# Optimization experiments

Hardware: AMD Instinct MI355X
Metric: run time of the kernel (lower is better)

## Reference

```python
import jax, jax.numpy as jnp
import numpy as np

D_MODEL = 1024
NUM_HEADS = 16
DEPTH = D_MODEL // NUM_HEADS
EPS = 1e-6


def setup_inputs() -> dict:
    key = jax.random.key(0)
    ks = jax.random.split(key, 9)
    B, S = 4, 2048
    scale = 1.0 / np.sqrt(D_MODEL)
    inp = {
        "inputs": jax.random.normal(ks[0], (B, S, D_MODEL), dtype=jnp.float32),
        "Wq": jax.random.normal(ks[1], (D_MODEL, D_MODEL), dtype=jnp.float32) * scale,
        "bq": jnp.zeros((D_MODEL,), dtype=jnp.float32),
        "Wk": jax.random.normal(ks[2], (D_MODEL, D_MODEL), dtype=jnp.float32) * scale,
        "bk": jnp.zeros((D_MODEL,), dtype=jnp.float32),
        "Wv": jax.random.normal(ks[3], (D_MODEL, D_MODEL), dtype=jnp.float32) * scale,
        "bv": jnp.zeros((D_MODEL,), dtype=jnp.float32),
        "Wo": jax.random.normal(ks[4], (D_MODEL, D_MODEL), dtype=jnp.float32) * scale,
        "bo": jnp.zeros((D_MODEL,), dtype=jnp.float32),
        "gamma": jnp.ones((D_MODEL,), dtype=jnp.float32),
        "beta": jnp.zeros((D_MODEL,), dtype=jnp.float32),
    }
    return inp


def _layer_norm(x, gamma, beta):
    mu = jnp.mean(x, axis=-1, keepdims=True)
    var = jnp.mean(jnp.square(x - mu), axis=-1, keepdims=True)
    return (x - mu) * jax.lax.rsqrt(var + EPS) * gamma + beta


def reference(inputs, Wq, bq, Wk, bk, Wv, bv, Wo, bo, gamma, beta):
    B, S, _ = inputs.shape
    # QKV projections, split heads: [B, H, S, depth]
    def split_heads(x):
        return x.reshape(B, S, NUM_HEADS, DEPTH).transpose(0, 2, 1, 3)

    q = split_heads(inputs @ Wq + bq)
    k = split_heads(inputs @ Wk + bk)
    v = split_heads(inputs @ Wv + bv)

    # scores: [B, H, S, S]
    scores = jnp.einsum("bhqd,bhkd->bhqk", q, k) / jnp.sqrt(
        jnp.asarray(DEPTH, dtype=inputs.dtype))
    attn = jax.nn.softmax(scores, axis=-1)  # dropout is identity in eval mode
    out = jnp.einsum("bhqk,bhkd->bhqd", attn, v)
    out = out.transpose(0, 2, 1, 3).reshape(B, S, D_MODEL)
    out = out @ Wo + bo  # dropout2 identity in eval mode
    return _layer_norm(inputs + out, gamma, beta)
```

## Files before the change

kernel.cpp:

```cpp
#include <hip/hip_runtime.h>
#include <hip/hip_bf16.h>


typedef __bf16 bf16;
typedef __bf16 bf16x4 __attribute__((ext_vector_type(4)));
typedef __bf16 bf16x8 __attribute__((ext_vector_type(8)));
typedef float floatx4 __attribute__((ext_vector_type(4)));

#define MFMA16(a, b, c) __builtin_amdgcn_mfma_f32_16x16x32_bf16((a), (b), (c), 0, 0, 0)

static __device__ __forceinline__ floatx4 vmax4(floatx4 a, floatx4 b) {
    floatx4 r;
    r[0] = fmaxf(a[0], b[0]); r[1] = fmaxf(a[1], b[1]);
    r[2] = fmaxf(a[2], b[2]); r[3] = fmaxf(a[3], b[3]);
    return r;
}

static __device__ __forceinline__ void gload16(const bf16* g, bf16* lds_base) {
    __builtin_amdgcn_global_load_lds(
        (__attribute__((address_space(1))) void*)(g),
        (__attribute__((address_space(3))) void*)(lds_base), 16, 0, 0);
}

__global__ __launch_bounds__(256) void convert_kernel(
    const float* __restrict__ x, bf16* __restrict__ xb)
{
    const int i = blockIdx.x * 256 + threadIdx.x;
    const float4 v = ((const float4*)x)[i];
    bf16x4 r;
    r[0] = (bf16)v.x; r[1] = (bf16)v.y; r[2] = (bf16)v.z; r[3] = (bf16)v.w;
    ((bf16x4*)xb)[i] = r;
}

__global__ __launch_bounds__(256) void transpose_kernel(
    const float* __restrict__ Wq, const float* __restrict__ Wk,
    const float* __restrict__ Wv, const float* __restrict__ Wo,
    bf16* __restrict__ WT, bf16* __restrict__ WoT)
{
    __shared__ float tile[32][33];
    const int z = blockIdx.z;
    const float* src = (z == 0) ? Wq : (z == 1) ? Wk : (z == 2) ? Wv : Wo;
    bf16* dst = (z < 3) ? (WT + (long)z * 1024 * 1024) : WoT;
    const int n0 = blockIdx.x * 32, k0 = blockIdx.y * 32;
    const int tx = threadIdx.x & 31, ty = threadIdx.x >> 5;
#pragma unroll
    for (int i = 0; i < 32; i += 8)
        tile[ty + i][tx] = src[(long)(k0 + ty + i) * 1024 + n0 + tx];
    __syncthreads();
#pragma unroll
    for (int i = 0; i < 32; i += 8)
        dst[(long)(n0 + ty + i) * 1024 + k0 + tx] = (bf16)tile[tx][ty + i];
}

template <int MODE>
__global__ __launch_bounds__(256, 2) void gemm_kernel(
    const bf16* __restrict__ A, const bf16* __restrict__ Bt,
    const float* __restrict__ b0, const float* __restrict__ b1,
    const float* __restrict__ b2, const float* __restrict__ X,
    bf16* __restrict__ Qo, bf16* __restrict__ Ko, bf16* __restrict__ Vto,
    bf16* __restrict__ Tmpb, int N, int K)
{
    constexpr int LDT = 32;
    constexpr int NBX = (MODE == 0) ? 24 : 8;
    constexpr int NWG = NBX * 64;
    constexpr int CPX = NWG / 8;
    __shared__ __align__(16) bf16 As[2][128 * LDT];
    __shared__ __align__(16) bf16 Bs[2][128 * LDT];
    const int t = threadIdx.x;
    const int lane = t & 63;
    const int w = t >> 6;
    const int wm = w >> 1, wn = w & 1;
    const int g = lane >> 4, c = lane & 15;

    const int id = blockIdx.y * NBX + blockIdx.x;
    const int swz = (id & 7) * CPX + (id >> 3);
    const int bm = (swz / NBX) * 128;
    const int bn = (swz % NBX) * 128;

    const bf16* asrc[2];
    const bf16* bsrc[2];
    int ldsoff[2];
#pragma unroll
    for (int i = 0; i < 2; ++i) {
        const int ch = (i * 4 + w) * 64 + lane;
        const int row = ch >> 2, col = ch & 3;
        asrc[i] = A + (long)(bm + row) * K + col * 8;
        bsrc[i] = Bt + (long)(bn + row) * K + col * 8;
        ldsoff[i] = (i * 4 + w) * 512;
    }

    floatx4 acc[4][4];
#pragma unroll
    for (int i = 0; i < 4; ++i)
#pragma unroll
        for (int j = 0; j < 4; ++j) acc[i][j] = floatx4{0.f, 0.f, 0.f, 0.f};

#pragma unroll
    for (int i = 0; i < 2; ++i) {
        gload16(asrc[i], &As[0][ldsoff[i]]);
        gload16(bsrc[i], &Bs[0][ldsoff[i]]);
    }

    int cur = 0;
    for (int k0 = 0; k0 < K; k0 += 32) {
        __syncthreads();
        if (k0 + 32 < K) {
#pragma unroll
            for (int i = 0; i < 2; ++i) {
                gload16(asrc[i] + k0 + 32, &As[cur ^ 1][ldsoff[i]]);
                gload16(bsrc[i] + k0 + 32, &Bs[cur ^ 1][ldsoff[i]]);
            }
        }
        bf16x8 af[4], bfv[4];
#pragma unroll
        for (int i = 0; i < 4; ++i)
            af[i] = *(const bf16x8*)&As[cur][(wm * 64 + i * 16 + c) * LDT + g * 8];
#pragma unroll
        for (int j = 0; j < 4; ++j)
            bfv[j] = *(const bf16x8*)&Bs[cur][(wn * 64 + j * 16 + c) * LDT + g * 8];
#pragma unroll
        for (int i = 0; i < 4; ++i)
#pragma unroll
            for (int j = 0; j < 4; ++j)
                acc[i][j] = MFMA16(af[i], bfv[j], acc[i][j]);
        cur ^= 1;
    }

    if (MODE == 0) {
#pragma unroll
        for (int j = 0; j < 4; ++j) {
            const int col = bn + wn * 64 + j * 16 + c;
            const int sec = col >> 10;
            const int nn = col & 1023;
            const int h = nn >> 6, dd = nn & 63;
            const float* bp = (sec == 0) ? b0 : (sec == 1) ? b1 : b2;
            const float bias = bp[nn];
#pragma unroll
            for (int i = 0; i < 4; ++i) {
                const int r0 = bm + wm * 64 + i * 16 + g * 4;
                if (sec == 2) {
                    bf16x4 pack;
#pragma unroll
                    for (int reg = 0; reg < 4; ++reg)
                        pack[reg] = (bf16)(acc[i][j][reg] + bias);
                    const int b_ = r0 >> 11, sr = r0 & 2047;
                    *(bf16x4*)&Vto[((long)(b_ * 16 + h) * 64 + dd) * 2048 + sr] = pack;
                } else {
#pragma unroll
                    for (int reg = 0; reg < 4; ++reg) {
                        const int r = r0 + reg;
                        const int b_ = r >> 11, sr = r & 2047;
                        const float v = acc[i][j][reg] + bias;
                        if (sec == 0)
                            Qo[((long)(b_ * 16 + h) * 2048 + sr) * 64 + dd] =
                                (bf16)(v * 0.18033688011112042f);
                        else
                            Ko[((long)(b_ * 16 + h) * 2048 + sr) * 64 + dd] = (bf16)v;
                    }
                }
            }
        }
    } else {
#pragma unroll
        for (int j = 0; j < 4; ++j) {
            const int col = bn + wn * 64 + j * 16 + c;
            const float bias = b0[col];
#pragma unroll
            for (int i = 0; i < 4; ++i) {
#pragma unroll
                for (int reg = 0; reg < 4; ++reg) {
                    const int r = bm + wm * 64 + i * 16 + g * 4 + reg;
                    Tmpb[(long)r * N + col] =
                        (bf16)(acc[i][j][reg] + bias + X[(long)r * N + col]);
                }
            }
        }
    }
}

__global__ __launch_bounds__(256, 2) void flash_kernel(
    const bf16* __restrict__ Q, const bf16* __restrict__ Kc,
    const bf16* __restrict__ Vt, bf16* __restrict__ O)
{
    constexpr int KSTR = 72;
    constexpr int VSTR = 72;
    constexpr int PSTR = 72;
    __shared__ __align__(16) bf16 Ks[64 * KSTR];
    __shared__ __align__(16) bf16 Vs[64 * VSTR];
    __shared__ __align__(16) bf16 Pl[4 * 32 * PSTR];
    const int t = threadIdx.x;
    const int lane = t & 63;
    const int w = t >> 6;
    const int g = lane >> 4, c = lane & 15;
    const int bh = blockIdx.x;
    const int b_ = bh >> 4, h = bh & 15;
    const bf16* Qp = Q + (long)bh * 2048 * 64;
    const bf16* Kp = Kc + (long)bh * 2048 * 64;
    const bf16* Vp = Vt + (long)bh * 64 * 2048;
    const int q0 = blockIdx.y * 128 + w * 32;
    bf16* Pw = Pl + w * 32 * PSTR;

    bf16x8 qf[2][2];
#pragma unroll
    for (int qs = 0; qs < 2; ++qs)
#pragma unroll
        for (int p = 0; p < 2; ++p)
            qf[qs][p] = *(const bf16x8*)(Qp + (long)(q0 + qs * 16 + c) * 64 + p * 32 + g * 8);

    float m_c[2] = {-1e30f, -1e30f};
    float l_c[2] = {0.f, 0.f};
    floatx4 o[2][4];
#pragma unroll
    for (int qs = 0; qs < 2; ++qs)
#pragma unroll
        for (int dd = 0; dd < 4; ++dd) o[qs][dd] = floatx4{0.f, 0.f, 0.f, 0.f};

    for (int kt = 0; kt < 32; ++kt) {
        __syncthreads();
        {
            uint4 kr[2], vr[2];
#pragma unroll
            for (int i = 0; i < 2; ++i) {
                const int idx = i * 256 + t;
                kr[i] = *(const uint4*)(Kp + (long)kt * 4096 + idx * 8);
                vr[i] = *(const uint4*)(Vp + (long)(idx >> 3) * 2048 + kt * 64 + (idx & 7) * 8);
            }
#pragma unroll
            for (int i = 0; i < 2; ++i) {
                const int idx = i * 256 + t;
                *(uint4*)&Ks[(idx >> 3) * KSTR + (idx & 7) * 8] = kr[i];
                *(uint4*)&Vs[(idx >> 3) * VSTR + (idx & 7) * 8] = vr[i];
            }
        }
        __syncthreads();

        floatx4 s[2][4];
#pragma unroll
        for (int ks = 0; ks < 4; ++ks) {
            bf16x8 kf0 = *(const bf16x8*)&Ks[(ks * 16 + c) * KSTR + g * 8];
            bf16x8 kf1 = *(const bf16x8*)&Ks[(ks * 16 + c) * KSTR + 32 + g * 8];
#pragma unroll
            for (int qs = 0; qs < 2; ++qs) {
                floatx4 z = floatx4{0.f, 0.f, 0.f, 0.f};
                z = MFMA16(kf0, qf[qs][0], z);
                z = MFMA16(kf1, qf[qs][1], z);
                s[qs][ks] = z;
            }
        }

#pragma unroll
        for (int qs = 0; qs < 2; ++qs) {
            floatx4 t0 = vmax4(vmax4(s[qs][0], s[qs][1]), vmax4(s[qs][2], s[qs][3]));
            float mx = fmaxf(fmaxf(t0[0], t0[1]), fmaxf(t0[2], t0[3]));
            mx = fmaxf(mx, __shfl_xor(mx, 16, 64));
            mx = fmaxf(mx, __shfl_xor(mx, 32, 64));
            const float mn = fmaxf(m_c[qs], mx);
            const float al = __builtin_amdgcn_exp2f(m_c[qs] - mn);
            m_c[qs] = mn;
            floatx4 a4 = floatx4{0.f, 0.f, 0.f, 0.f};
#pragma unroll
            for (int ks = 0; ks < 4; ++ks) {
#pragma unroll
                for (int r = 0; r < 4; ++r)
                    s[qs][ks][r] = __builtin_amdgcn_exp2f(s[qs][ks][r] - mn);
                a4 += s[qs][ks];
            }
            float rs = (a4[0] + a4[1]) + (a4[2] + a4[3]);
            rs += __shfl_xor(rs, 16, 64);
            rs += __shfl_xor(rs, 32, 64);
            l_c[qs] = l_c[qs] * al + rs;
#pragma unroll
            for (int dd = 0; dd < 4; ++dd)
#pragma unroll
                for (int r = 0; r < 4; ++r) o[qs][dd][r] *= al;
#pragma unroll
            for (int ks = 0; ks < 4; ++ks) {
                bf16x4 pk;
#pragma unroll
                for (int r = 0; r < 4; ++r) pk[r] = (bf16)s[qs][ks][r];
                *(bf16x4*)&Pw[(qs * 16 + c) * PSTR + ks * 16 + g * 4] = pk;
            }
        }
        asm volatile("s_waitcnt lgkmcnt(0)" ::: "memory");
#pragma unroll
        for (int kk = 0; kk < 2; ++kk) {
            bf16x8 pf0 = *(const bf16x8*)&Pw[(0 + c) * PSTR + kk * 32 + g * 8];
            bf16x8 pf1 = *(const bf16x8*)&Pw[(16 + c) * PSTR + kk * 32 + g * 8];
#pragma unroll
            for (int dd = 0; dd < 4; ++dd) {
                bf16x8 vf = *(const bf16x8*)&Vs[(dd * 16 + c) * VSTR + kk * 32 + g * 8];
                o[0][dd] = MFMA16(vf, pf0, o[0][dd]);
                o[1][dd] = MFMA16(vf, pf1, o[1][dd]);
            }
        }
    }

#pragma unroll
    for (int qs = 0; qs < 2; ++qs) {
        const float linv = 1.0f / l_c[qs];
        const int q = q0 + qs * 16 + c;
#pragma unroll
        for (int dd = 0; dd < 4; ++dd) {
            bf16x4 pk;
#pragma unroll
            for (int r = 0; r < 4; ++r) pk[r] = (bf16)(o[qs][dd][r] * linv);
            *(bf16x4*)&O[((long)b_ * 2048 + q) * 1024 + h * 64 + dd * 16 + g * 4] = pk;
        }
    }
}

__global__ __launch_bounds__(256, 2) void ln_kernel(
    const bf16* __restrict__ Tmp, const float* __restrict__ gamma,
    const float* __restrict__ beta, float* __restrict__ out)
{
    const int row = blockIdx.x;
    const int t = threadIdx.x;
    const int lane = t & 63, w = t >> 6;
    const bf16x4 vb = ((const bf16x4*)(Tmp + (long)row * 1024))[t];
    const float xv[4] = {(float)vb[0], (float)vb[1], (float)vb[2], (float)vb[3]};
    float s = xv[0] + xv[1] + xv[2] + xv[3];
    float ss = xv[0] * xv[0] + xv[1] * xv[1] + xv[2] * xv[2] + xv[3] * xv[3];
#pragma unroll
    for (int off = 1; off < 64; off <<= 1) {
        s += __shfl_xor(s, off, 64);
        ss += __shfl_xor(ss, off, 64);
    }
    __shared__ float sb[4], ssb[4];
    if (lane == 0) { sb[w] = s; ssb[w] = ss; }
    __syncthreads();
    s = sb[0] + sb[1] + sb[2] + sb[3];
    ss = ssb[0] + ssb[1] + ssb[2] + ssb[3];
    const float mu = s * (1.0f / 1024.0f);
    const float var = ss * (1.0f / 1024.0f) - mu * mu;
    const float inv = rsqrtf(var + 1e-6f);
    const float4 gm = ((const float4*)gamma)[t];
    const float4 bt = ((const float4*)beta)[t];
    float4 r;
    r.x = (xv[0] - mu) * inv * gm.x + bt.x;
    r.y = (xv[1] - mu) * inv * gm.y + bt.y;
    r.z = (xv[2] - mu) * inv * gm.z + bt.z;
    r.w = (xv[3] - mu) * inv * gm.w + bt.w;
    ((float4*)(out + (long)row * 1024))[t] = r;
}

extern "C" void kernel_launch(void* const* d_in, const int* in_sizes, int n_in,
                              void* d_out, int out_size, void* d_ws, size_t ws_size,
                              hipStream_t stream)
{
    const float* x     = (const float*)d_in[0];
    const float* Wq    = (const float*)d_in[1];
    const float* bq    = (const float*)d_in[2];
    const float* Wk    = (const float*)d_in[3];
    const float* bk    = (const float*)d_in[4];
    const float* Wv    = (const float*)d_in[5];
    const float* bv    = (const float*)d_in[6];
    const float* Wo    = (const float*)d_in[7];
    const float* bo    = (const float*)d_in[8];
    const float* gamma = (const float*)d_in[9];
    const float* beta  = (const float*)d_in[10];
    float* out = (float*)d_out;

    char* ws = (char*)d_ws;
    bf16* xb   = (bf16*)(ws);
    bf16* WT   = (bf16*)(ws + 16777216);
    bf16* Qb   = (bf16*)(ws + 23068672);
    bf16* Kb   = (bf16*)(ws + 39845888);
    bf16* WoT  = (bf16*)(ws + 56623104);
    bf16* Tmpb = (bf16*)(ws);
    bf16* Vtb  = (bf16*)d_out;
    bf16* Ob   = (bf16*)((char*)d_out + 16777216);

    convert_kernel<<<8192, 256, 0, stream>>>(x, xb);
    transpose_kernel<<<dim3(32, 32, 4), 256, 0, stream>>>(Wq, Wk, Wv, Wo, WT, WoT);
    gemm_kernel<0><<<dim3(24, 64), 256, 0, stream>>>(
        xb, WT, bq, bk, bv, nullptr, Qb, Kb, Vtb, nullptr, 3072, 1024);
    flash_kernel<<<dim3(64, 16), 256, 0, stream>>>(Qb, Kb, Vtb, Ob);
    gemm_kernel<1><<<dim3(8, 64), 256, 0, stream>>>(
        Ob, WoT, bo, nullptr, nullptr, x, nullptr, nullptr, nullptr, Tmpb, 1024, 1024);
    ln_kernel<<<8192, 256, 0, stream>>>(Tmpb, gamma, beta, out);
}
```

Measured before the change: 340.1 us.

## Restructure flash attention with 32x32 MFMA, register P, double-buffered async K/V loads

Rewrites the attention kernel to use 32x32x16 bf16 MFMA tiles, so each wave handles 32 query rows with one softmax state. The P matrix is rearranged into the operand layout with cross-half-wave shuffles instead of a round trip through LDS. K/V tiles are now double-buffered and loaded with async global_load_lds into an XOR-swizzled unpadded layout, which overlaps the next tile's load with the current compute and removes one barrier per iteration. The cost is heavier register use for the 16-wide accumulators, and correctness depends on the async loads being complete before the barrier.

Result: faster. 325.0 us (-4.4%).

```diff
diff --git a/kernel.cpp b/kernel.cpp
--- a/kernel.cpp
+++ b/kernel.cpp
@@ -3,18 +3,14 @@
 
 
 typedef __bf16 bf16;
+typedef __bf16 bf16x2 __attribute__((ext_vector_type(2)));
 typedef __bf16 bf16x4 __attribute__((ext_vector_type(4)));
 typedef __bf16 bf16x8 __attribute__((ext_vector_type(8)));
 typedef float floatx4 __attribute__((ext_vector_type(4)));
+typedef float floatx16 __attribute__((ext_vector_type(16)));
 
 #define MFMA16(a, b, c) __builtin_amdgcn_mfma_f32_16x16x32_bf16((a), (b), (c), 0, 0, 0)
-
-static __device__ __forceinline__ floatx4 vmax4(floatx4 a, floatx4 b) {
-    floatx4 r;
-    r[0] = fmaxf(a[0], b[0]); r[1] = fmaxf(a[1], b[1]);
-    r[2] = fmaxf(a[2], b[2]); r[3] = fmaxf(a[3], b[3]);
-    return r;
-}
+#define MFMA32(a, b, c) __builtin_amdgcn_mfma_f32_32x32x16_bf16((a), (b), (c), 0, 0, 0)
 
 static __device__ __forceinline__ void gload16(const bf16* g, bf16* lds_base) {
     __builtin_amdgcn_global_load_lds(
@@ -182,131 +178,167 @@
     const bf16* __restrict__ Q, const bf16* __restrict__ Kc,
     const bf16* __restrict__ Vt, bf16* __restrict__ O)
 {
-    constexpr int KSTR = 72;
-    constexpr int VSTR = 72;
-    constexpr int PSTR = 72;
-    __shared__ __align__(16) bf16 Ks[64 * KSTR];
-    __shared__ __align__(16) bf16 Vs[64 * VSTR];
-    __shared__ __align__(16) bf16 Pl[4 * 32 * PSTR];
+    __shared__ __align__(16) bf16 KVs[2][2][64 * 64];
     const int t = threadIdx.x;
     const int lane = t & 63;
     const int w = t >> 6;
-    const int g = lane >> 4, c = lane & 15;
+    const int l31 = lane & 31, hw = lane >> 5;
     const int bh = blockIdx.x;
     const int b_ = bh >> 4, h = bh & 15;
     const bf16* Qp = Q + (long)bh * 2048 * 64;
     const bf16* Kp = Kc + (long)bh * 2048 * 64;
     const bf16* Vp = Vt + (long)bh * 64 * 2048;
-    const int q0 = blockIdx.y * 128 + w * 32;
-    bf16* Pw = Pl + w * 32 * PSTR;
-
-    bf16x8 qf[2][2];
-#pragma unroll
-    for (int qs = 0; qs < 2; ++qs)
-#pragma unroll
-        for (int p = 0; p < 2; ++p)
-            qf[qs][p] = *(const bf16x8*)(Qp + (long)(q0 + qs * 16 + c) * 64 + p * 32 + g * 8);
-
-    float m_c[2] = {-1e30f, -1e30f};
-    float l_c[2] = {0.f, 0.f};
-    floatx4 o[2][4];
-#pragma unroll
-    for (int qs = 0; qs < 2; ++qs)
-#pragma unroll
-        for (int dd = 0; dd < 4; ++dd) o[qs][dd] = floatx4{0.f, 0.f, 0.f, 0.f};
+    const int q0w = blockIdx.y * 128 + w * 32;
+
+    const bf16* ksrc[2];
+    const bf16* vsrc[2];
+    int ldsoff[2];
+#pragma unroll
+    for (int i = 0; i < 2; ++i) {
+        const int ch = (i * 4 + w) * 64 + lane;
+        const int row = ch >> 3, col = ch & 7;
+        const int sw = col ^ (row & 7);
+        ksrc[i] = Kp + (long)(row * 8 + sw) * 8;
+        vsrc[i] = Vp + (long)row * 2048 + sw * 8;
+        ldsoff[i] = (i * 4 + w) * 512;
+    }
+
+    bf16x8 qf[4];
+#pragma unroll
+    for (int sl = 0; sl < 4; ++sl)
+        qf[sl] = *(const bf16x8*)(Qp + (long)(q0w + l31) * 64 + sl * 16 + hw * 8);
+
+    float m_c = -1e30f;
+    float l_c = 0.f;
+    floatx16 o32[2];
+#pragma unroll
+    for (int dt = 0; dt < 2; ++dt)
+#pragma unroll
+        for (int i = 0; i < 16; ++i) o32[dt][i] = 0.f;
+
+#pragma unroll
+    for (int i = 0; i < 2; ++i) {
+        gload16(ksrc[i], &KVs[0][0][ldsoff[i]]);
+        gload16(vsrc[i], &KVs[0][1][ldsoff[i]]);
+    }
 
     for (int kt = 0; kt < 32; ++kt) {
         __syncthreads();
+        const int cur = kt & 1;
+        if (kt + 1 < 32) {
+#pragma unroll
+            for (int i = 0; i < 2; ++i) {
+                gload16(ksrc[i] + (long)(kt + 1) * 4096, &KVs[cur ^ 1][0][ldsoff[i]]);
+                gload16(vsrc[i] + (long)(kt + 1) * 64,   &KVs[cur ^ 1][1][ldsoff[i]]);
+            }
+        }
+        const bf16* KsB = KVs[cur][0];
+        const bf16* VsB = KVs[cur][1];
+
+        floatx16 s32[2];
+#pragma unroll
+        for (int kt_ = 0; kt_ < 2; ++kt_)
+#pragma unroll
+            for (int i = 0; i < 16; ++i) s32[kt_][i] = 0.f;
+#pragma unroll
+        for (int sl = 0; sl < 4; ++sl) {
+            const int x = sl * 2 + hw;
+            const int r0 = l31, r1 = 32 + l31;
+            const int xs = x ^ (r0 & 7);
+            bf16x8 kf0 = *(const bf16x8*)&KsB[r0 * 64 + (xs << 3)];
+            bf16x8 kf1 = *(const bf16x8*)&KsB[r1 * 64 + (xs << 3)];
+            s32[0] = MFMA32(kf0, qf[sl], s32[0]);
+            s32[1] = MFMA32(kf1, qf[sl], s32[1]);
+        }
+
+        float mx;
         {
-            uint4 kr[2], vr[2];
-#pragma unroll
-            for (int i = 0; i < 2; ++i) {
-                const int idx = i * 256 + t;
-                kr[i] = *(const uint4*)(Kp + (long)kt * 4096 + idx * 8);
-                vr[i] = *(const uint4*)(Vp + (long)(idx >> 3) * 2048 + kt * 64 + (idx & 7) * 8);
-            }
-#pragma unroll
-            for (int i = 0; i < 2; ++i) {
-                const int idx = i * 256 + t;
-                *(uint4*)&Ks[(idx >> 3) * KSTR + (idx & 7) * 8] = kr[i];
-                *(uint4*)&Vs[(idx >> 3) * VSTR + (idx & 7) * 8] = vr[i];
-            }
-        }
-        __syncthreads();
-
-        floatx4 s[2][4];
-#pragma unroll
-        for (int ks = 0; ks < 4; ++ks) {
-            bf16x8 kf0 = *(const bf16x8*)&Ks[(ks * 16 + c) * KSTR + g * 8];
-            bf16x8 kf1 = *(const bf16x8*)&Ks[(ks * 16 + c) * KSTR + 32 + g * 8];
-#pragma unroll
-            for (int qs = 0; qs < 2; ++qs) {
-                floatx4 z = floatx4{0.f, 0.f, 0.f, 0.f};
-                z = MFMA16(kf0, qf[qs][0], z);
-                z = MFMA16(kf1, qf[qs][1], z);
-                s[qs][ks] = z;
-            }
-        }
-
-#pragma unroll
-        for (int qs = 0; qs < 2; ++qs) {
-            floatx4 t0 = vmax4(vmax4(s[qs][0], s[qs][1]), vmax4(s[qs][2], s[qs][3]));
-            float mx = fmaxf(fmaxf(t0[0], t0[1]), fmaxf(t0[2], t0[3]));
-            mx = fmaxf(mx, __shfl_xor(mx, 16, 64));
-            mx = fmaxf(mx, __shfl_xor(mx, 32, 64));
-            const float mn = fmaxf(m_c[qs], mx);
-            const float al = __builtin_amdgcn_exp2f(m_c[qs] - mn);
-            m_c[qs] = mn;
-            floatx4 a4 = floatx4{0.f, 0.f, 0.f, 0.f};
-#pragma unroll
-            for (int ks = 0; ks < 4; ++ks) {
-#pragma unroll
-                for (int r = 0; r < 4; ++r)
-                    s[qs][ks][r] = __builtin_amdgcn_exp2f(s[qs][ks][r] - mn);
-                a4 += s[qs][ks];
-            }
-            float rs = (a4[0] + a4[1]) + (a4[2] + a4[3]);
-            rs += __shfl_xor(rs, 16, 64);
-            rs += __shfl_xor(rs, 32, 64);
-            l_c[qs] = l_c[qs] * al + rs;
-#pragma unroll
-            for (int dd = 0; dd < 4; ++dd)
-#pragma unroll
-                for (int r = 0; r < 4; ++r) o[qs][dd][r] *= al;
-#pragma unroll
-            for (int ks = 0; ks < 4; ++ks) {
-                bf16x4 pk;
-#pragma unroll
-                for (int r = 0; r < 4; ++r) pk[r] = (bf16)s[qs][ks][r];
-                *(bf16x4*)&Pw[(qs * 16 + c) * PSTR + ks * 16 + g * 4] = pk;
-            }
-        }
-        asm volatile("s_waitcnt lgkmcnt(0)" ::: "memory");
-#pragma unroll
-        for (int kk = 0; kk < 2; ++kk) {
-            bf16x8 pf0 = *(const bf16x8*)&Pw[(0 + c) * PSTR + kk * 32 + g * 8];
-            bf16x8 pf1 = *(const bf16x8*)&Pw[(16 + c) * PSTR + kk * 32 + g * 8];
-#pragma unroll
-            for (int dd = 0; dd < 4; ++dd) {
-                bf16x8 vf = *(const bf16x8*)&Vs[(dd * 16 + c) * VSTR + kk * 32 + g * 8];
-                o[0][dd] = MFMA16(vf, pf0, o[0][dd]);
-                o[1][dd] = MFMA16(vf, pf1, o[1][dd]);
-            }
-        }
-    }
-
-#pragma unroll
-    for (int qs = 0; qs < 2; ++qs) {
-        const float linv = 1.0f / l_c[qs];
-        const int q = q0 + qs * 16 + c;
-#pragma unroll
-        for (int dd = 0; dd < 4; ++dd) {
+            float tm[16];
+#pragma unroll
+            for (int i = 0; i < 16; ++i) tm[i] = fmaxf(s32[0][i], s32[1][i]);
+            float a0 = fmaxf(fmaxf(tm[0], tm[1]), fmaxf(tm[2], tm[3]));
+            float a1 = fmaxf(fmaxf(tm[4], tm[5]), fmaxf(tm[6], tm[7]));
+            float a2 = fmaxf(fmaxf(tm[8], tm[9]), fmaxf(tm[10], tm[11]));
+            float a3 = fmaxf(fmaxf(tm[12], tm[13]), fmaxf(tm[14], tm[15]));
+            mx = fmaxf(fmaxf(a0, a1), fmaxf(a2, a3));
+        }
+        mx = fmaxf(mx, __shfl_xor(mx, 32, 64));
+        const float mn = fmaxf(m_c, mx);
+        const float al = __builtin_amdgcn_exp2f(m_c - mn);
+        m_c = mn;
+        float r0s = 0.f, r1s = 0.f, r2s = 0.f, r3s = 0.f;
+#pragma unroll
+        for (int kt_ = 0; kt_ < 2; ++kt_) {
+#pragma unroll
+            for (int i = 0; i < 16; i += 4) {
+                s32[kt_][i + 0] = __builtin_amdgcn_exp2f(s32[kt_][i + 0] - mn);
+                s32[kt_][i + 1] = __builtin_amdgcn_exp2f(s32[kt_][i + 1] - mn);
+                s32[kt_][i + 2] = __builtin_amdgcn_exp2f(s32[kt_][i + 2] - mn);
+                s32[kt_][i + 3] = __builtin_amdgcn_exp2f(s32[kt_][i + 3] - mn);
+                r0s += s32[kt_][i + 0]; r1s += s32[kt_][i + 1];
+                r2s += s32[kt_][i + 2]; r3s += s32[kt_][i + 3];
+            }
+        }
+        float rs = (r0s + r1s) + (r2s + r3s);
+        rs += __shfl_xor(rs, 32, 64);
+        l_c = l_c * al + rs;
+#pragma unroll
+        for (int dt = 0; dt < 2; ++dt)
+#pragma unroll
+            for (int i = 0; i < 16; ++i) o32[dt][i] *= al;
+
+        uint32_t dpk[2][8];
+#pragma unroll
+        for (int kt_ = 0; kt_ < 2; ++kt_)
+#pragma unroll
+            for (int u = 0; u < 8; ++u) {
+                bf16x2 p2;
+                p2[0] = (bf16)s32[kt_][2 * u];
+                p2[1] = (bf16)s32[kt_][2 * u + 1];
+                dpk[kt_][u] = __builtin_bit_cast(uint32_t, p2);
+            }
+
+        bf16x8 pb[4];
+#pragma unroll
+        for (int sl = 0; sl < 4; ++sl) {
+            const int kt_ = sl >> 1;
+            const int ub = (sl & 1) * 4;
+            const uint32_t eA = hw ? dpk[kt_][ub + 0] : dpk[kt_][ub + 2];
+            const uint32_t eB = hw ? dpk[kt_][ub + 1] : dpk[kt_][ub + 3];
+            const uint32_t rA = (uint32_t)__shfl_xor((int)eA, 32, 64);
+            const uint32_t rB = (uint32_t)__shfl_xor((int)eB, 32, 64);
+            uint4 fr;
+            if (hw == 0)
+                fr = make_uint4(dpk[kt_][ub + 0], dpk[kt_][ub + 1], rA, rB);
+            else
+                fr = make_uint4(rA, rB, dpk[kt_][ub + 2], dpk[kt_][ub + 3]);
+            pb[sl] = __builtin_bit_cast(bf16x8, fr);
+        }
+
+#pragma unroll
+        for (int sl = 0; sl < 4; ++sl) {
+            const int x = sl * 2 + hw;
+#pragma unroll
+            for (int dt = 0; dt < 2; ++dt) {
+                const int row = dt * 32 + l31;
+                bf16x8 vf = *(const bf16x8*)&VsB[row * 64 + ((x ^ (row & 7)) << 3)];
+                o32[dt] = MFMA32(vf, pb[sl], o32[dt]);
+            }
+        }
+    }
+
+    const float linv = 1.0f / l_c;
+    const int q = q0w + l31;
+#pragma unroll
+    for (int dt = 0; dt < 2; ++dt)
+#pragma unroll
+        for (int rg = 0; rg < 4; ++rg) {
             bf16x4 pk;
 #pragma unroll
-            for (int r = 0; r < 4; ++r) pk[r] = (bf16)(o[qs][dd][r] * linv);
-            *(bf16x4*)&O[((long)b_ * 2048 + q) * 1024 + h * 64 + dd * 16 + g * 4] = pk;
-        }
-    }
+            for (int r = 0; r < 4; ++r) pk[r] = (bf16)(o32[dt][rg * 4 + r] * linv);
+            const int d0 = dt * 32 + rg * 8 + hw * 4;
+            *(bf16x4*)&O[((long)b_ * 2048 + q) * 1024 + h * 64 + d0] = pk;
+        }
 }
 
 __global__ __launch_bounds__(256, 2) void ln_kernel(
```
